# Performance work log

Hardware: AMD Instinct MI355X
Metric: run time of the kernel (lower is better)

The kernel has to match this reference:

```python
import jax, jax.numpy as jnp
import numpy as np

N_NODES = 100000


def gcn_conv(x, edge_index, W, b):
    """PyG GCNConv: out = D^-1/2 (A+I) D^-1/2 (X W) + b, edge weights = 1."""
    n = x.shape[0]
    h = x @ W  # [N, F_out]
    row, col = edge_index[0], edge_index[1]  # source -> target
    ones = jnp.ones(row.shape[0], dtype=x.dtype)
    # degree on A + I (self loop contributes 1)
    deg = jax.ops.segment_sum(ones, col, num_segments=n) + 1.0
    dinv = jax.lax.rsqrt(deg)  # deg >= 1 so no inf
    norm = dinv[row] * dinv[col]  # [E]
    agg = jax.ops.segment_sum(h[row] * norm[:, None], col, num_segments=n)
    agg = agg + h * (dinv * dinv)[:, None]  # self-loop term
    return agg + b


def setup_inputs() -> dict:
    key = jax.random.key(0)
    ks = jax.random.split(key, 8)
    E = 3200000
    F_in, H, C = 128, 16, 2
    x = jax.random.normal(ks[0], (N_NODES, F_in), dtype=jnp.float32)
    edge_index = jax.random.randint(ks[1], (2, E), 0, N_NODES, dtype=jnp.int64)
    W1 = jax.random.normal(ks[2], (F_in, H), dtype=jnp.float32) * (1.0 / np.sqrt(F_in))
    b1 = jnp.zeros((H,), jnp.float32)
    W2 = jax.random.normal(ks[3], (H, H), dtype=jnp.float32) * (1.0 / np.sqrt(H))
    b2 = jnp.zeros((H,), jnp.float32)
    fc1_W = jax.random.normal(ks[4], (2 * H, H), dtype=jnp.float32) * (1.0 / np.sqrt(2 * H))
    fc1_b = jnp.zeros((H,), jnp.float32)
    fc2_W = jax.random.normal(ks[5], (H, C), dtype=jnp.float32) * (1.0 / np.sqrt(H))
    fc2_b = jnp.zeros((C,), jnp.float32)
    return {"x": x, "edge_index": edge_index, "W1": W1, "b1": b1, "W2": W2,
            "b2": b2, "fc1_W": fc1_W, "fc1_b": fc1_b, "fc2_W": fc2_W, "fc2_b": fc2_b}


def reference(x, edge_index, W1, b1, W2, b2, fc1_W, fc1_b, fc2_W, fc2_b):
    h = jax.nn.relu(gcn_conv(x, edge_index, W1, b1))
    h = jax.nn.relu(gcn_conv(h, edge_index, W2, b2))
    row, col = edge_index[0], edge_index[1]
    ef = jnp.concatenate([h[row], h[col]], axis=1)  # [E, 32]
    ef = jax.nn.relu(ef @ fc1_W + fc1_b)
    logits = ef @ fc2_W + fc2_b  # [E, 2]
    return jax.nn.log_softmax(logits, axis=1)
```

## Files before the change

### kernel.cpp

```cpp
#include <hip/hip_runtime.h>
#include <hip/hip_fp16.h>
#include <cstdint>
#include <cstddef>

#define F_IN 128
#define HID 16
#define NBUK 1024
#define NPB  128
#define CHUNK 8192
#define CHUNK2 16384

typedef float f4v __attribute__((ext_vector_type(4)));
typedef float f2v __attribute__((ext_vector_type(2)));
typedef int   i2v __attribute__((ext_vector_type(2)));
typedef int   i4v __attribute__((ext_vector_type(4)));

__global__ void k_detect(const int* __restrict__ eidx, int* __restrict__ flag) {
    if (blockIdx.x == 0 && threadIdx.x == 0) {
        int all0 = 1;
        for (int i = 0; i < 64; ++i) {
            if (eidx[2 * i + 1] != 0) { all0 = 0; break; }
        }
        *flag = all0;
    }
}

__device__ __forceinline__ int ld_idx_nt(const int* __restrict__ p, int e, int is64) {
    return is64 ? __builtin_nontemporal_load(&p[2 * e])
                : __builtin_nontemporal_load(&p[e]);
}

__launch_bounds__(256)
__global__ void k_bhist(const int* __restrict__ eidx, int E,
                        const int* __restrict__ flag, int* __restrict__ ghist) {
    __shared__ int lh[NBUK];
    int t = threadIdx.x;
    for (int i = t; i < NBUK; i += 256) lh[i] = 0;
    __syncthreads();
    int base = blockIdx.x * CHUNK;
    int cnt = min(CHUNK, E - base);
    int is64 = *flag;
    const int* colp = eidx + ((size_t)E << is64);
    for (int i = t; i < cnt; i += 256)
        atomicAdd(&lh[ld_idx_nt(colp, base + i, is64) >> 7], 1);
    __syncthreads();
    for (int i = t; i < NBUK; i += 256)
        if (lh[i]) atomicAdd(&ghist[i], lh[i]);
}

__global__ void k_bscan(const int* __restrict__ ghist, int E,
                        int* __restrict__ boff, int* __restrict__ gcur) {
    __shared__ int s[NBUK];
    int t = threadIdx.x;
    int v = ghist[t];
    s[t] = v;
    __syncthreads();
    for (int off = 1; off < NBUK; off <<= 1) {
        int a = (t >= off) ? s[t - off] : 0;
        __syncthreads();
        s[t] += a;
        __syncthreads();
    }
    int excl = s[t] - v;
    boff[t] = excl;
    gcur[t] = excl;
    if (t == NBUK - 1) boff[NBUK] = E;
}

__launch_bounds__(512)
__global__ void k_bscatter(const int* __restrict__ eidx, int E,
                           const int* __restrict__ flag,
                           int* __restrict__ gcur, uint32_t* __restrict__ pairs) {
    __shared__ int lh[NBUK];
    __shared__ int lcur[NBUK];
    int t = threadIdx.x;
    for (int i = t; i < NBUK; i += 512) lh[i] = 0;
    __syncthreads();
    int base = blockIdx.x * CHUNK2;
    int cnt = min(CHUNK2, E - base);
    int is64 = *flag;
    const int* rowp = eidx;
    const int* colp = eidx + ((size_t)E << is64);
    for (int i = t; i < cnt; i += 512)
        atomicAdd(&lh[ld_idx_nt(colp, base + i, is64) >> 7], 1);
    __syncthreads();
    for (int i = t; i < NBUK; i += 512) {
        int c = lh[i];
        lcur[i] = c ? atomicAdd(&gcur[i], c) : 0;
    }
    __syncthreads();
    for (int i = t; i < cnt; i += 512) {
        int e = base + i;
        int c = ld_idx_nt(colp, e, is64);
        int r = ld_idx_nt(rowp, e, is64);
        int buk = c >> 7;
        int pos = atomicAdd(&lcur[buk], 1);
        pairs[pos] = (uint32_t)r | ((uint32_t)(c & (NPB - 1)) << 20);
    }
}

__launch_bounds__(256)
__global__ void k_bsort(const uint32_t* __restrict__ pairs, const int* __restrict__ boff,
                        int* __restrict__ srcs, int* __restrict__ noff,
                        float* __restrict__ dinv, int n) {
    __shared__ int cnt[NPB];
    __shared__ int scn[NPB];
    int t = threadIdx.x;
    int b = blockIdx.x;
    if (t < NPB) cnt[t] = 0;
    __syncthreads();
    int beg = boff[b], end = boff[b + 1];
    for (int k = beg + t; k < end; k += 256)
        atomicAdd(&cnt[pairs[k] >> 20], 1);
    __syncthreads();
    if (t < NPB) scn[t] = cnt[t];
    __syncthreads();
    for (int off = 1; off < NPB; off <<= 1) {
        int v = 0;
        if (t < NPB && t >= off) v = scn[t - off];
        __syncthreads();
        if (t < NPB) scn[t] += v;
        __syncthreads();
    }
    if (t < NPB) {
        int node = b * NPB + t;
        int excl = scn[t] - cnt[t];
        if (node <= n) noff[node] = beg + excl;
        if (node < n)  dinv[node] = rsqrtf((float)cnt[t] + 1.0f);
        cnt[t] = beg + excl;
    }
    __syncthreads();
    for (int k = beg + t; k < end; k += 256) {
        uint32_t p = pairs[k];
        int pos = atomicAdd(&cnt[p >> 20], 1);
        srcs[pos] = (int)(p & 0xFFFFF);
    }
}

__launch_bounds__(256)
__global__ void k_gemm1(const float* __restrict__ x, const float* __restrict__ W1,
                        const float* __restrict__ dinv, __half* __restrict__ hs, int n) {
    __shared__ float Wt[16 * 132];
    for (int i = threadIdx.x; i < F_IN * HID; i += 256) {
        int k = i >> 4, j = i & 15;
        Wt[j * 132 + k] = W1[i];
    }
    __syncthreads();
    int row = blockIdx.x * 16 + (threadIdx.x >> 4);
    int j = threadIdx.x & 15;
    if (row >= n) return;
    const f4v* xr = (const f4v*)(x + (size_t)row * F_IN);
    float acc = 0.f;
#pragma unroll
    for (int kk = 0; kk < 32; ++kk) {
        f4v xv = __builtin_nontemporal_load(&xr[kk]);
        float4 wv = *(const float4*)&Wt[j * 132 + 4 * kk];
        acc += xv.x * wv.x + xv.y * wv.y + xv.z * wv.z + xv.w * wv.w;
    }
    hs[(size_t)row * HID + j] = __float2half(acc * dinv[row]);
}

template <int EPI>
__launch_bounds__(256)
__global__ void k_layer(const int* __restrict__ srcs, const int* __restrict__ noff,
                        const __half* __restrict__ hs, const float* __restrict__ dinv,
                        const float* __restrict__ bias, const float* __restrict__ Wnext,
                        __half* __restrict__ out0, __half* __restrict__ out1) {
    __shared__ float Ws[512];
    __shared__ float bs[16];
    __shared__ float srow[16 * 17];
    int t = threadIdx.x;
    int nw = (EPI == 0) ? 256 : 512;
    for (int i = t; i < nw; i += 256) Ws[i] = Wnext[i];
    if (t < 16) bs[t] = bias[t];
    __syncthreads();

    int i = blockIdx.x * 16 + (t >> 4);
    int j = t & 15;
    int beg = noff[i], end = noff[i + 1];
    float acc = __half2float(hs[(size_t)i * HID + j]);

    int kb = beg;
    for (; kb + 16 <= end; kb += 16) {
        int idx = __builtin_nontemporal_load(&srcs[kb + j]);
#pragma unroll
        for (int m = 0; m < 16; ++m) {
            int r = __shfl(idx, m, 16);
            acc += __half2float(hs[(size_t)r * HID + j]);
        }
    }
    if (kb < end) {
        int lim = end - kb;
        int idx = srcs[kb + ((j < lim) ? j : (lim - 1))];
        for (int m = 0; m < lim; ++m) {
            int r = __shfl(idx, m, 16);
            acc += __half2float(hs[(size_t)r * HID + j]);
        }
    }

    float di = dinv[i];
    float hrelu = fmaxf(acc * di + bs[j], 0.f);
    int ln = t >> 4;
    srow[ln * 17 + j] = hrelu;
    __syncthreads();
    float a0 = 0.f, a1 = 0.f;
#pragma unroll
    for (int k = 0; k < 16; ++k) {
        float hv = srow[ln * 17 + k];
        a0 += hv * Ws[k * 16 + j];
        if (EPI == 1) a1 += hv * Ws[(16 + k) * 16 + j];
    }
    if (EPI == 0) {
        out0[(size_t)i * HID + j] = __float2half(a0 * di);
    } else {
        out0[(size_t)i * HID + j] = __float2half(a0);
        out1[(size_t)i * HID + j] = __float2half(a1);
    }
}

__launch_bounds__(256)
__global__ void k_edge(const int* __restrict__ eidx, int E,
                       const int* __restrict__ flag,
                       const __half* __restrict__ u, const __half* __restrict__ v,
                       const float* __restrict__ fc1b, const float* __restrict__ fc2W,
                       const float* __restrict__ fc2b, float* __restrict__ out) {
    __shared__ float b1s[16], W2s[32], b2s[2];
    if (threadIdx.x < 16) b1s[threadIdx.x] = fc1b[threadIdx.x];
    if (threadIdx.x < 32) W2s[threadIdx.x] = fc2W[threadIdx.x];
    if (threadIdx.x < 2) b2s[threadIdx.x] = fc2b[threadIdx.x];
    __syncthreads();
    int g = blockIdx.x * blockDim.x + threadIdx.x;
    int e0 = 2 * g;
    if (e0 >= E) return;
    bool has1 = (e0 + 1 < E);
    int is64 = *flag;
    const int* rowp = eidx;
    const int* colp = eidx + ((size_t)E << is64);
    int r0, c0, r1, c1;
    if (is64) {
        i4v rw = __builtin_nontemporal_load((const i4v*)(rowp + 2 * (size_t)e0));
        i4v cw = __builtin_nontemporal_load((const i4v*)(colp + 2 * (size_t)e0));
        r0 = rw.x; r1 = rw.z; c0 = cw.x; c1 = cw.z;
    } else {
        i2v rw = __builtin_nontemporal_load((const i2v*)(rowp + e0));
        i2v cw = __builtin_nontemporal_load((const i2v*)(colp + e0));
        r0 = rw.x; r1 = rw.y; c0 = cw.x; c1 = cw.y;
    }
    if (!has1) { r1 = r0; c1 = c0; }
    const uint4* p0 = (const uint4*)(u + (size_t)r0 * HID);
    const uint4* q0 = (const uint4*)(v + (size_t)c0 * HID);
    const uint4* p1 = (const uint4*)(u + (size_t)r1 * HID);
    const uint4* q1 = (const uint4*)(v + (size_t)c1 * HID);
    uint4 U0a = p0[0], U0b = p0[1], V0a = q0[0], V0b = q0[1];
    uint4 U1a = p1[0], U1b = p1[1], V1a = q1[0], V1b = q1[1];

#define PROC(l0, l1, uw, vw, jb)                                                \
    {                                                                           \
        float2 fu = __half22float2(*(__half2*)&(uw));                           \
        float2 fv = __half22float2(*(__half2*)&(vw));                           \
        float z = fmaxf(fu.x + fv.x + b1s[jb], 0.f);                            \
        l0 += z * W2s[2 * (jb)]; l1 += z * W2s[2 * (jb) + 1];                   \
        z = fmaxf(fu.y + fv.y + b1s[(jb) + 1], 0.f);                            \
        l0 += z * W2s[2 * (jb) + 2]; l1 += z * W2s[2 * (jb) + 3];               \
    }
    float a0 = b2s[0], a1 = b2s[1];
    PROC(a0, a1, U0a.x, V0a.x, 0) PROC(a0, a1, U0a.y, V0a.y, 2)
    PROC(a0, a1, U0a.z, V0a.z, 4) PROC(a0, a1, U0a.w, V0a.w, 6)
    PROC(a0, a1, U0b.x, V0b.x, 8) PROC(a0, a1, U0b.y, V0b.y, 10)
    PROC(a0, a1, U0b.z, V0b.z, 12) PROC(a0, a1, U0b.w, V0b.w, 14)
    float b0 = b2s[0], b1v = b2s[1];
    PROC(b0, b1v, U1a.x, V1a.x, 0) PROC(b0, b1v, U1a.y, V1a.y, 2)
    PROC(b0, b1v, U1a.z, V1a.z, 4) PROC(b0, b1v, U1a.w, V1a.w, 6)
    PROC(b0, b1v, U1b.x, V1b.x, 8) PROC(b0, b1v, U1b.y, V1b.y, 10)
    PROC(b0, b1v, U1b.z, V1b.z, 12) PROC(b0, b1v, U1b.w, V1b.w, 14)
#undef PROC
    float m0 = fmaxf(a0, a1);
    float lse0 = m0 + __logf(__expf(a0 - m0) + __expf(a1 - m0));
    float m1 = fmaxf(b0, b1v);
    float lse1 = m1 + __logf(__expf(b0 - m1) + __expf(b1v - m1));
    if (has1) {
        f4v res; res.x = a0 - lse0; res.y = a1 - lse0;
        res.z = b0 - lse1; res.w = b1v - lse1;
        __builtin_nontemporal_store(res, (f4v*)(out + 2 * (size_t)e0));
    } else {
        f2v res; res.x = a0 - lse0; res.y = a1 - lse0;
        __builtin_nontemporal_store(res, (f2v*)(out + 2 * (size_t)e0));
    }
}

static inline size_t rnd4(size_t v) { return (v + 3) & ~(size_t)3; }

extern "C" void kernel_launch(void* const* d_in, const int* in_sizes, int n_in,
                              void* d_out, int out_size, void* d_ws, size_t ws_size,
                              hipStream_t stream) {
    const float* x    = (const float*)d_in[0];
    const int*   eidx = (const int*)d_in[1];
    const float* W1   = (const float*)d_in[2];
    const float* b1   = (const float*)d_in[3];
    const float* W2   = (const float*)d_in[4];
    const float* b2   = (const float*)d_in[5];
    const float* fc1W = (const float*)d_in[6];
    const float* fc1b = (const float*)d_in[7];
    const float* fc2W = (const float*)d_in[8];
    const float* fc2b = (const float*)d_in[9];

    const int n = in_sizes[0] / F_IN;
    const int E = in_sizes[1] / 2;
    const int NBLK_HIST = (E + CHUNK - 1) / CHUNK;
    const int NBLK_SCAT = (E + CHUNK2 - 1) / CHUNK2;
    const int NBLK_BUK  = (n + NPB - 1) / NPB;

    float* ws = (float*)d_ws;
    size_t a = 0;
    float*    dinv  = ws + a;              a += rnd4(n);
    uint32_t* pairs = (uint32_t*)(ws + a); a += rnd4(E);
    int*      srcs  = (int*)(ws + a);      a += rnd4(E);
    int*      noff  = (int*)(ws + a);      a += rnd4(n + 1);
    int*      boff  = (int*)(ws + a);      a += rnd4(NBUK + 1);
    int*      gcur  = (int*)(ws + a);      a += NBUK;
    int*      ghist = (int*)(ws + a);      a += NBUK;
    int*      flag  = (int*)(ws + a);      a += 4;
    __half*   hs1   = (__half*)(ws + a);   a += rnd4((size_t)n * HID / 2);
    __half*   hs2   = (__half*)(ws + a);   a += rnd4((size_t)n * HID / 2);
    __half*   ubuf  = (__half*)(ws + a);   a += rnd4((size_t)n * HID / 2);
    __half*   vbuf  = (__half*)(ws + a);   a += rnd4((size_t)n * HID / 2);
    float* out = (float*)d_out;

    k_detect<<<1, 64, 0, stream>>>(eidx, flag);

    (void)hipMemsetAsync(ghist, 0, NBUK * sizeof(int), stream);
    k_bhist<<<NBLK_HIST, 256, 0, stream>>>(eidx, E, flag, ghist);
    k_bscan<<<1, NBUK, 0, stream>>>(ghist, E, boff, gcur);
    k_bscatter<<<NBLK_SCAT, 512, 0, stream>>>(eidx, E, flag, gcur, pairs);
    k_bsort<<<NBLK_BUK, 256, 0, stream>>>(pairs, boff, srcs, noff, dinv, n);

    k_gemm1<<<(n + 15) / 16, 256, 0, stream>>>(x, W1, dinv, hs1, n);

    k_layer<0><<<n / 16, 256, 0, stream>>>(srcs, noff, hs1, dinv, b1, W2, hs2, nullptr);
    k_layer<1><<<n / 16, 256, 0, stream>>>(srcs, noff, hs2, dinv, b2, fc1W, ubuf, vbuf);
    {
        int npair = (E + 1) / 2;
        k_edge<<<(npair + 255) / 256, 256, 0, stream>>>(eidx, E, flag, ubuf, vbuf,
                                                        fc1b, fc2W, fc2b, out);
    }
}
```

Before: 315.7 us.

## Compute edge MLP with MFMA on gathered h2 instead of precomputed per-node projections

Layer 2 now writes only the relu'd hidden features instead of projecting them through both halves of fc1. The edge kernel gathers h2 for source and target and runs fc1 as a 16x16x32 f16 MFMA per group of 16 edges, then reduces fc2 with cross-lane shuffles before log-softmax. This drops the per-node projection step and one node buffer. In exchange the edge kernel does more arithmetic, many shuffles and one write lane per four edges, and fc1 weights are rounded to half precision.

```diff
diff --git a/kernel.cpp b/kernel.cpp
--- a/kernel.cpp
+++ b/kernel.cpp
@@ -14,6 +14,7 @@
 typedef float f2v __attribute__((ext_vector_type(2)));
 typedef int   i2v __attribute__((ext_vector_type(2)));
 typedef int   i4v __attribute__((ext_vector_type(4)));
+typedef _Float16 h8 __attribute__((ext_vector_type(8)));
 
 __global__ void k_detect(const int* __restrict__ eidx, int* __restrict__ flag) {
     if (blockIdx.x == 0 && threadIdx.x == 0) {
@@ -165,13 +166,12 @@
 __global__ void k_layer(const int* __restrict__ srcs, const int* __restrict__ noff,
                         const __half* __restrict__ hs, const float* __restrict__ dinv,
                         const float* __restrict__ bias, const float* __restrict__ Wnext,
-                        __half* __restrict__ out0, __half* __restrict__ out1) {
-    __shared__ float Ws[512];
+                        __half* __restrict__ out0) {
+    __shared__ float Ws[256];
     __shared__ float bs[16];
     __shared__ float srow[16 * 17];
     int t = threadIdx.x;
-    int nw = (EPI == 0) ? 256 : 512;
-    for (int i = t; i < nw; i += 256) Ws[i] = Wnext[i];
+    if (EPI == 0) { if (t < 256) Ws[t] = Wnext[t]; }
     if (t < 16) bs[t] = bias[t];
     __syncthreads();
 
@@ -200,91 +200,89 @@
 
     float di = dinv[i];
     float hrelu = fmaxf(acc * di + bs[j], 0.f);
+    if (EPI == 1) {
+        out0[(size_t)i * HID + j] = __float2half(hrelu);
+        return;
+    }
     int ln = t >> 4;
     srow[ln * 17 + j] = hrelu;
     __syncthreads();
-    float a0 = 0.f, a1 = 0.f;
-#pragma unroll
-    for (int k = 0; k < 16; ++k) {
-        float hv = srow[ln * 17 + k];
-        a0 += hv * Ws[k * 16 + j];
-        if (EPI == 1) a1 += hv * Ws[(16 + k) * 16 + j];
-    }
-    if (EPI == 0) {
-        out0[(size_t)i * HID + j] = __float2half(a0 * di);
-    } else {
-        out0[(size_t)i * HID + j] = __float2half(a0);
-        out1[(size_t)i * HID + j] = __float2half(a1);
-    }
-}
-
+    float a0 = 0.f;
+#pragma unroll
+    for (int k = 0; k < 16; ++k) a0 += srow[ln * 17 + k] * Ws[k * 16 + j];
+    out0[(size_t)i * HID + j] = __float2half(a0 * di);
+}
+
+#define EDGE_ITER 8
 __launch_bounds__(256)
 __global__ void k_edge(const int* __restrict__ eidx, int E,
                        const int* __restrict__ flag,
-                       const __half* __restrict__ u, const __half* __restrict__ v,
-                       const float* __restrict__ fc1b, const float* __restrict__ fc2W,
-                       const float* __restrict__ fc2b, float* __restrict__ out) {
-    __shared__ float b1s[16], W2s[32], b2s[2];
-    if (threadIdx.x < 16) b1s[threadIdx.x] = fc1b[threadIdx.x];
-    if (threadIdx.x < 32) W2s[threadIdx.x] = fc2W[threadIdx.x];
-    if (threadIdx.x < 2) b2s[threadIdx.x] = fc2b[threadIdx.x];
-    __syncthreads();
-    int g = blockIdx.x * blockDim.x + threadIdx.x;
-    int e0 = 2 * g;
-    if (e0 >= E) return;
-    bool has1 = (e0 + 1 < E);
+                       const _Float16* __restrict__ h2,
+                       const float* __restrict__ fc1W, const float* __restrict__ fc1b,
+                       const float* __restrict__ fc2W, const float* __restrict__ fc2b,
+                       float* __restrict__ out) {
+    int t = threadIdx.x;
+    int l = t & 63;
+    int wv = t >> 6;
+    int m = l & 15;
+    int kb = l >> 4;
+    int side = kb >> 1;
+    int part = kb & 1;
+
+    h8 bf;
+#pragma unroll
+    for (int j = 0; j < 8; ++j)
+        bf[j] = (_Float16)fc1W[(8 * kb + j) * 16 + m];
+    float b1v = fc1b[m];
+    f4v cinit; cinit.x = b1v; cinit.y = b1v; cinit.z = b1v; cinit.w = b1v;
+    float w20 = fc2W[2 * m], w21 = fc2W[2 * m + 1];
+    float b20 = fc2b[0], b21 = fc2b[1];
+
     int is64 = *flag;
     const int* rowp = eidx;
     const int* colp = eidx + ((size_t)E << is64);
-    int r0, c0, r1, c1;
-    if (is64) {
-        i4v rw = __builtin_nontemporal_load((const i4v*)(rowp + 2 * (size_t)e0));
-        i4v cw = __builtin_nontemporal_load((const i4v*)(colp + 2 * (size_t)e0));
-        r0 = rw.x; r1 = rw.z; c0 = cw.x; c1 = cw.z;
-    } else {
-        i2v rw = __builtin_nontemporal_load((const i2v*)(rowp + e0));
-        i2v cw = __builtin_nontemporal_load((const i2v*)(colp + e0));
-        r0 = rw.x; r1 = rw.y; c0 = cw.x; c1 = cw.y;
-    }
-    if (!has1) { r1 = r0; c1 = c0; }
-    const uint4* p0 = (const uint4*)(u + (size_t)r0 * HID);
-    const uint4* q0 = (const uint4*)(v + (size_t)c0 * HID);
-    const uint4* p1 = (const uint4*)(u + (size_t)r1 * HID);
-    const uint4* q1 = (const uint4*)(v + (size_t)c1 * HID);
-    uint4 U0a = p0[0], U0b = p0[1], V0a = q0[0], V0b = q0[1];
-    uint4 U1a = p1[0], U1b = p1[1], V1a = q1[0], V1b = q1[1];
-
-#define PROC(l0, l1, uw, vw, jb)                                                \
-    {                                                                           \
-        float2 fu = __half22float2(*(__half2*)&(uw));                           \
-        float2 fv = __half22float2(*(__half2*)&(vw));                           \
-        float z = fmaxf(fu.x + fv.x + b1s[jb], 0.f);                            \
-        l0 += z * W2s[2 * (jb)]; l1 += z * W2s[2 * (jb) + 1];                   \
-        z = fmaxf(fu.y + fv.y + b1s[(jb) + 1], 0.f);                            \
-        l0 += z * W2s[2 * (jb) + 2]; l1 += z * W2s[2 * (jb) + 3];               \
-    }
-    float a0 = b2s[0], a1 = b2s[1];
-    PROC(a0, a1, U0a.x, V0a.x, 0) PROC(a0, a1, U0a.y, V0a.y, 2)
-    PROC(a0, a1, U0a.z, V0a.z, 4) PROC(a0, a1, U0a.w, V0a.w, 6)
-    PROC(a0, a1, U0b.x, V0b.x, 8) PROC(a0, a1, U0b.y, V0b.y, 10)
-    PROC(a0, a1, U0b.z, V0b.z, 12) PROC(a0, a1, U0b.w, V0b.w, 14)
-    float b0 = b2s[0], b1v = b2s[1];
-    PROC(b0, b1v, U1a.x, V1a.x, 0) PROC(b0, b1v, U1a.y, V1a.y, 2)
-    PROC(b0, b1v, U1a.z, V1a.z, 4) PROC(b0, b1v, U1a.w, V1a.w, 6)
-    PROC(b0, b1v, U1b.x, V1b.x, 8) PROC(b0, b1v, U1b.y, V1b.y, 10)
-    PROC(b0, b1v, U1b.z, V1b.z, 12) PROC(b0, b1v, U1b.w, V1b.w, 14)
-#undef PROC
-    float m0 = fmaxf(a0, a1);
-    float lse0 = m0 + __logf(__expf(a0 - m0) + __expf(a1 - m0));
-    float m1 = fmaxf(b0, b1v);
-    float lse1 = m1 + __logf(__expf(b0 - m1) + __expf(b1v - m1));
-    if (has1) {
-        f4v res; res.x = a0 - lse0; res.y = a1 - lse0;
-        res.z = b0 - lse1; res.w = b1v - lse1;
-        __builtin_nontemporal_store(res, (f4v*)(out + 2 * (size_t)e0));
-    } else {
-        f2v res; res.x = a0 - lse0; res.y = a1 - lse0;
-        __builtin_nontemporal_store(res, (f2v*)(out + 2 * (size_t)e0));
+    const int* idxp = side ? colp : rowp;
+
+    for (int it = 0; it < EDGE_ITER; ++it) {
+        int grp = (blockIdx.x * EDGE_ITER + it) * 4 + wv;
+        int base = grp * 16;
+        if (base >= E) return;
+        int eA = base + m;
+        if (eA >= E) eA = E - 1;
+        int node = ld_idx_nt(idxp, eA, is64);
+        h8 av = *(const h8*)(h2 + (size_t)node * HID + part * 8);
+        f4v z = __builtin_amdgcn_mfma_f32_16x16x32_f16(av, bf, cinit, 0, 0, 0);
+        float l0[4], l1[4];
+#pragma unroll
+        for (int q = 0; q < 4; ++q) {
+            float zr = fmaxf(z[q], 0.f);
+            float v0 = zr * w20, v1 = zr * w21;
+#pragma unroll
+            for (int msk = 1; msk < 16; msk <<= 1) {
+                v0 += __shfl_xor(v0, msk);
+                v1 += __shfl_xor(v1, msk);
+            }
+            float a = b20 + v0, b = b21 + v1;
+            float mm = fmaxf(a, b);
+            float lse = mm + __logf(__expf(a - mm) + __expf(b - mm));
+            l0[q] = a - lse; l1[q] = b - lse;
+        }
+        if (m == 0) {
+            int e0 = base + kb * 4;
+            if (e0 + 3 < E) {
+                f4v o1; o1.x = l0[0]; o1.y = l1[0]; o1.z = l0[1]; o1.w = l1[1];
+                f4v o2; o2.x = l0[2]; o2.y = l1[2]; o2.z = l0[3]; o2.w = l1[3];
+                __builtin_nontemporal_store(o1, (f4v*)(out + 2 * (size_t)e0));
+                __builtin_nontemporal_store(o2, (f4v*)(out + 2 * (size_t)e0 + 4));
+            } else {
+                for (int q = 0; q < 4; ++q) {
+                    if (e0 + q < E) {
+                        f2v o; o.x = l0[q]; o.y = l1[q];
+                        __builtin_nontemporal_store(o, (f2v*)(out + 2 * (size_t)(e0 + q)));
+                    }
+                }
+            }
+        }
     }
 }
 
@@ -322,8 +320,7 @@
     int*      flag  = (int*)(ws + a);      a += 4;
     __half*   hs1   = (__half*)(ws + a);   a += rnd4((size_t)n * HID / 2);
     __half*   hs2   = (__half*)(ws + a);   a += rnd4((size_t)n * HID / 2);
-    __half*   ubuf  = (__half*)(ws + a);   a += rnd4((size_t)n * HID / 2);
-    __half*   vbuf  = (__half*)(ws + a);   a += rnd4((size_t)n * HID / 2);
+    __half*   h2b   = (__half*)(ws + a);   a += rnd4((size_t)n * HID / 2);
     float* out = (float*)d_out;
 
     k_detect<<<1, 64, 0, stream>>>(eidx, flag);
@@ -336,11 +333,12 @@
 
     k_gemm1<<<(n + 15) / 16, 256, 0, stream>>>(x, W1, dinv, hs1, n);
 
-    k_layer<0><<<n / 16, 256, 0, stream>>>(srcs, noff, hs1, dinv, b1, W2, hs2, nullptr);
-    k_layer<1><<<n / 16, 256, 0, stream>>>(srcs, noff, hs2, dinv, b2, fc1W, ubuf, vbuf);
+    k_layer<0><<<n / 16, 256, 0, stream>>>(srcs, noff, hs1, dinv, b1, W2, hs2);
+    k_layer<1><<<n / 16, 256, 0, stream>>>(srcs, noff, hs2, dinv, b2, nullptr, h2b);
     {
-        int npair = (E + 1) / 2;
-        k_edge<<<(npair + 255) / 256, 256, 0, stream>>>(eidx, E, flag, ubuf, vbuf,
-                                                        fc1b, fc2W, fc2b, out);
-    }
-}
+        int ngrp = (E + 15) / 16;
+        int nblk = (ngrp + 4 * EDGE_ITER - 1) / (4 * EDGE_ITER);
+        k_edge<<<nblk, 256, 0, stream>>>(eidx, E, flag, (const _Float16*)h2b,
+                                         fc1W, fc1b, fc2W, fc2b, out);
+    }
+}
```

Result: no change. 319.6 us (+1.2%).
